# Optimization experiments

Measured on AMD Instinct MI355X. Metric: run time of the kernel, lower is better.

## Reference

```python
import jax, jax.numpy as jnp
import numpy as np

K = 512      # per-token feature dim (also per-head dim in this module)
H = 8        # heads
B = 2
T = 2048


def setup_inputs() -> dict:
    key = jax.random.key(0)
    ks = jax.random.split(key, 6)
    s = 1.0 / np.sqrt(K)
    x = jax.random.normal(ks[0], (B, T, K), dtype=jnp.float32)
    # torch Linear(k, k*heads, bias=False): y = x @ W with W stored here as [in, out]
    Wq = jax.random.uniform(ks[1], (K, K * H), dtype=jnp.float32, minval=-s, maxval=s)
    Wk = jax.random.uniform(ks[2], (K, K * H), dtype=jnp.float32, minval=-s, maxval=s)
    Wv = jax.random.uniform(ks[3], (K, K * H), dtype=jnp.float32, minval=-s, maxval=s)
    su = 1.0 / np.sqrt(K * H)
    Wu = jax.random.uniform(ks[4], (K * H, K), dtype=jnp.float32, minval=-su, maxval=su)
    bu = jax.random.uniform(ks[5], (K,), dtype=jnp.float32, minval=-su, maxval=su)
    return {"x": x, "Wq": Wq, "Wk": Wk, "Wv": Wv, "Wu": Wu, "bu": bu}


def reference(x, Wq, Wk, Wv, Wu, bu):
    b, t, k = x.shape
    h = H
    # project and split heads: [b, t, h, k] -> [b, h, t, k]
    q = (x @ Wq).reshape(b, t, h, k).transpose(0, 2, 1, 3)
    kk = (x @ Wk).reshape(b, t, h, k).transpose(0, 2, 1, 3)
    v = (x @ Wv).reshape(b, t, h, k).transpose(0, 2, 1, 3)
    scale = k ** (-0.25)  # applied to both q and k, matching source
    dot = jnp.einsum('bhqd,bhkd->bhqk', q * scale, kk * scale)
    attn = jax.nn.softmax(dot, axis=-1)
    out = jnp.einsum('bhqk,bhkd->bhqd', attn, v)          # [b, h, t, k]
    out = out.transpose(0, 2, 1, 3).reshape(b, t, h * k)   # [b, t, h*k]
    return out @ Wu + bu
```

## Files before the change

### kernel.cpp

```cpp
#include <hip/hip_runtime.h>

typedef unsigned short u16;
typedef unsigned short ushort8 __attribute__((ext_vector_type(8)));
typedef unsigned short us4 __attribute__((ext_vector_type(4)));
typedef __bf16 bf16x8 __attribute__((ext_vector_type(8)));
typedef float f32x4 __attribute__((ext_vector_type(4)));

#define DEV static __device__ __forceinline__

DEV u16 f2bf(float f) {
    unsigned int u = __builtin_bit_cast(unsigned int, f);
    u += 0x7FFFu + ((u >> 16) & 1u);
    return (u16)(u >> 16);
}

DEV f32x4 mfma16(ushort8 a, ushort8 b, f32x4 c) {
    return __builtin_amdgcn_mfma_f32_16x16x32_bf16((bf16x8)a, (bf16x8)b, c, 0, 0, 0);
}

DEV void gload_lds16(const void* g, void* l) {
    __builtin_amdgcn_global_load_lds(
        (const __attribute__((address_space(1))) void*)g,
        (__attribute__((address_space(3))) void*)l, 16, 0, 0);
}

__global__ void prep_kernel(const float* __restrict__ x,
                            const float* __restrict__ Wq, const float* __restrict__ Wk,
                            const float* __restrict__ Wv, const float* __restrict__ Wu,
                            u16* __restrict__ xb, u16* __restrict__ Wqt, u16* __restrict__ Wut) {
    __shared__ u16 tile[64][72];
    const int bid = blockIdx.x;

    if (bid < 2048) {
        int i = (bid * 256 + threadIdx.x) * 4;
        float4 f = *(const float4*)(x + i);
        us4 o;
        o.x = f2bf(f.x); o.y = f2bf(f.y); o.z = f2bf(f.z); o.w = f2bf(f.w);
        *(us4*)(xb + i) = o;
        return;
    }

    const float* in;
    u16* out;
    int R, C, c0, r0;
    if (bid < 3584) {
        int j = bid - 2048;
        int z = j >> 9, rem = j & 511;
        in = (z == 0) ? Wq : (z == 1) ? Wk : Wv;
        out = Wqt + (size_t)z * 2097152;
        R = 512; C = 4096;
        c0 = (rem & 63) << 6; r0 = (rem >> 6) << 6;
    } else {
        int k = bid - 3584;
        in = Wu; out = Wut;
        R = 4096; C = 512;
        c0 = (k & 7) << 6; r0 = (k >> 3) << 6;
    }
    int tx = threadIdx.x & 63, ty = threadIdx.x >> 6;
    for (int i = 0; i < 64; i += 4) {
        int r = i + ty;
        tile[r][tx] = f2bf(in[(size_t)(r0 + r) * C + c0 + tx]);
    }
    __syncthreads();
    for (int i = 0; i < 64; i += 4) {
        int r = i + ty;
        out[(size_t)(c0 + r) * R + r0 + tx] = tile[tx][r];
    }
}

__launch_bounds__(256, 3)
__global__ void gemm_qkv(const u16* __restrict__ A, const u16* __restrict__ Btbase,
                         float s2, u16* __restrict__ outbase, u16* __restrict__ vtb) {
    __shared__ u16 Asub[128 * 32];
    __shared__ u16 Bsub[128 * 32];
    const int Kc = 512;
    const u16* Bt = Btbase + (size_t)blockIdx.z * 2097152;
    u16* out = outbase + (size_t)blockIdx.z * 16777216;
    const float scale = (blockIdx.z == 0) ? s2 : 1.0f;

    const int tid = threadIdx.x, lane = tid & 63, wv = tid >> 6;
    const int bm = blockIdx.y << 7, bn = blockIdx.x << 7;
    const int wr = (wv >> 1) << 6, wc = (wv & 1) << 6;
    const int lr = lane & 15, hi = lane >> 4;

    f32x4 acc[4][4] = {};

    int off0 = (wv * 2048 + lane * 16) >> 1;
    int row0 = off0 >> 5, k0e = off0 & 31;
    int off1 = off0 + 512;
    int row1 = off1 >> 5, k1e = off1 & 31;

    const u16* Ag0 = A + (size_t)(bm + row0) * Kc + k0e;
    const u16* Ag1 = A + (size_t)(bm + row1) * Kc + k1e;
    const u16* Bg0 = Bt + (size_t)(bn + row0) * Kc + k0e;
    const u16* Bg1 = Bt + (size_t)(bn + row1) * Kc + k1e;

    for (int kk = 0; kk < Kc; kk += 32) {
        __syncthreads();
        gload_lds16(Ag0 + kk, &Asub[wv * 1024]);
        gload_lds16(Ag1 + kk, &Asub[wv * 1024 + 512]);
        gload_lds16(Bg0 + kk, &Bsub[wv * 1024]);
        gload_lds16(Bg1 + kk, &Bsub[wv * 1024 + 512]);
        __syncthreads();

        ushort8 a[4], b[4];
#pragma unroll
        for (int m = 0; m < 4; ++m)
            a[m] = *(const ushort8*)&Asub[(wr + m * 16 + lr) * 32 + hi * 8];
#pragma unroll
        for (int n = 0; n < 4; ++n)
            b[n] = *(const ushort8*)&Bsub[(wc + n * 16 + lr) * 32 + hi * 8];
#pragma unroll
        for (int m = 0; m < 4; ++m)
#pragma unroll
            for (int n = 0; n < 4; ++n)
                acc[m][n] = mfma16(a[m], b[n], acc[m][n]);
    }

    if (blockIdx.z == 2) {
#pragma unroll
        for (int m = 0; m < 4; ++m)
#pragma unroll
            for (int n = 0; n < 4; ++n) {
                int row0v = bm + wr + m * 16 + hi * 4;
                int col   = bn + wc + n * 16 + lr;
                int b = row0v >> 11, t0 = row0v & 2047;
                int h = col >> 9, d = col & 511;
                us4 pk;
#pragma unroll
                for (int r = 0; r < 4; ++r) pk[r] = f2bf(acc[m][n][r]);
                *(us4*)&vtb[(((size_t)(b * 8 + h) * 512 + d) << 11) + t0] = pk;
            }
    } else {
#pragma unroll
        for (int m = 0; m < 4; ++m)
#pragma unroll
            for (int n = 0; n < 4; ++n)
#pragma unroll
                for (int r = 0; r < 4; ++r) {
                    int row = bm + wr + m * 16 + hi * 4 + r;
                    int col = bn + wc + n * 16 + lr;
                    float v = acc[m][n][r] * scale;
                    size_t dst = ((size_t)((row >> 11) * 8 + (col >> 9)) * 2048 + (row & 2047)) * 512
                                 + (col & 511);
                    out[dst] = f2bf(v);
                }
    }
}

__launch_bounds__(256, 3)
__global__ void gemm_final(const u16* __restrict__ A, const u16* __restrict__ Bt,
                           const float* __restrict__ bias, float* __restrict__ out, int Kc) {
    __shared__ u16 Asub[128 * 32];
    __shared__ u16 Bsub[64 * 32];
    const int tid = threadIdx.x, lane = tid & 63, wv = tid >> 6;
    const int bm = blockIdx.y << 7, bn = blockIdx.x << 6;
    const int wr = (wv >> 1) << 6, wc = (wv & 1) << 5;
    const int lr = lane & 15, hi = lane >> 4;

    f32x4 acc[4][2] = {};

    const u16* gsrc[3];
    u16* ldst[3];
#pragma unroll
    for (int j = 0; j < 3; ++j) {
        int g = wv * 3 + j;
        int off = g * 512 + lane * 8;
        if (g < 8) {
            int row = off >> 5, k = off & 31;
            gsrc[j] = A + (size_t)(bm + row) * Kc + k;
            ldst[j] = &Asub[g * 512];
        } else {
            int off2 = off - 4096;
            int row = off2 >> 5, k = off2 & 31;
            gsrc[j] = Bt + (size_t)(bn + row) * Kc + k;
            ldst[j] = &Bsub[(g - 8) * 512];
        }
    }

    for (int kk = 0; kk < Kc; kk += 32) {
        __syncthreads();
#pragma unroll
        for (int j = 0; j < 3; ++j) gload_lds16(gsrc[j] + kk, ldst[j]);
        __syncthreads();

        ushort8 a[4], b[2];
#pragma unroll
        for (int m = 0; m < 4; ++m)
            a[m] = *(const ushort8*)&Asub[(wr + m * 16 + lr) * 32 + hi * 8];
#pragma unroll
        for (int n = 0; n < 2; ++n)
            b[n] = *(const ushort8*)&Bsub[(wc + n * 16 + lr) * 32 + hi * 8];
#pragma unroll
        for (int m = 0; m < 4; ++m)
#pragma unroll
            for (int n = 0; n < 2; ++n)
                acc[m][n] = mfma16(a[m], b[n], acc[m][n]);
    }

#pragma unroll
    for (int m = 0; m < 4; ++m)
#pragma unroll
        for (int n = 0; n < 2; ++n)
#pragma unroll
            for (int r = 0; r < 4; ++r) {
                int row = bm + wr + m * 16 + hi * 4 + r;
                int col = bn + wc + n * 16 + lr;
                out[(size_t)row * 512 + col] = acc[m][n][r] + bias[col];
            }
}

__launch_bounds__(512, 2)
__global__ void attn_kernel(const u16* __restrict__ Q, const u16* __restrict__ K,
                            const u16* __restrict__ Vt, u16* __restrict__ O) {
    __shared__ u16 Klds[2][32 * 512];
    __shared__ u16 Plds[2][128 * 40];
    __shared__ __align__(16) float red[2][128];
    __shared__ __align__(16) float lred[128];
    __shared__ int rflag[2][8];

    const int tid = threadIdx.x, lane = tid & 63, wv = tid >> 6;
    const int lr = lane & 15, hi = lane >> 4;
    const int qh = wv >> 2, ds = wv & 3;

    const int flat = blockIdx.x;
    const int nid = (flat & 7) * 32 + (flat >> 3);
    const int bh = nid >> 4;
    const int q0 = (nid & 15) << 7;

    ushort8 qf[16];
    {
        const char* Qg = (const char*)(Q + ((size_t)bh * 2048 + q0 + wv * 16 + lr) * 512) + hi * 16;
#pragma unroll
        for (int ks = 0; ks < 16; ++ks) qf[ks] = *(const ushort8*)(Qg + ks * 64);
    }

    f32x4 acc[4][8] = {};
    float mrun = -1e30f, lrun = 0.f;

    const char* Kg = (const char*)(K + (size_t)bh * 2048 * 512);
    const char* Vg = (const char*)(Vt + (size_t)bh * 512 * 2048);

    auto s_phase = [&](const char* Kb, f32x4& s0, f32x4& s1) {
        s0 = (f32x4){0.f, 0.f, 0.f, 0.f};
        s1 = (f32x4){0.f, 0.f, 0.f, 0.f};
#pragma unroll
        for (int ks = 0; ks < 16; ++ks) {
            int swz = (ks * 64 + hi * 16) ^ ((lr & 7) << 4);
            ushort8 kf0 = *(const ushort8*)(Kb + lr * 1024 + swz);
            ushort8 kf1 = *(const ushort8*)(Kb + (lr + 16) * 1024 + swz);
            s0 = mfma16(kf0, qf[ks], s0);
            s1 = mfma16(kf1, qf[ks], s1);
        }
    };

    auto softmax_store = [&](const f32x4& s0, const f32x4& s1, int pcb) {
        float mx = fmaxf(fmaxf(fmaxf(s0[0], s0[1]), fmaxf(s0[2], s0[3])),
                         fmaxf(fmaxf(s1[0], s1[1]), fmaxf(s1[2], s1[3])));
        mx = fmaxf(mx, __shfl_xor(mx, 16));
        mx = fmaxf(mx, __shfl_xor(mx, 32));
        float a = 1.0f;
        bool upd = false;
        if (mx > mrun + 11.5f) { a = exp2f(mrun - mx); mrun = mx; upd = true; }
        float p[8];
#pragma unroll
        for (int r = 0; r < 4; ++r) {
            p[r]     = exp2f(s0[r] - mrun);
            p[4 + r] = exp2f(s1[r] - mrun);
        }
        float ps = ((p[0] + p[1]) + (p[2] + p[3])) + ((p[4] + p[5]) + (p[6] + p[7]));
        ps += __shfl_xor(ps, 16);
        ps += __shfl_xor(ps, 32);
        lrun = lrun * a + ps;

        const int qr = wv * 16 + lr;
        char* Pb = (char*)&Plds[pcb][0] + qr * 80;
        uint2 w01, w23;
        w01.x = (unsigned)f2bf(p[0]) | ((unsigned)f2bf(p[1]) << 16);
        w01.y = (unsigned)f2bf(p[2]) | ((unsigned)f2bf(p[3]) << 16);
        w23.x = (unsigned)f2bf(p[4]) | ((unsigned)f2bf(p[5]) << 16);
        w23.y = (unsigned)f2bf(p[6]) | ((unsigned)f2bf(p[7]) << 16);
        *(uint2*)(Pb + hi * 8) = w01;
        *(uint2*)(Pb + 32 + hi * 8) = w23;
        if (hi == 0) red[pcb][qr] = a;
        if (lane == 0) rflag[pcb][wv] = __any(upd) ? 1 : 0;
    };

    auto pv_phase = [&](int pcb, int ktv) {
        int anyupd = rflag[pcb][0] | rflag[pcb][1] | rflag[pcb][2] | rflag[pcb][3]
                   | rflag[pcb][4] | rflag[pcb][5] | rflag[pcb][6] | rflag[pcb][7];
        if (anyupd) {
#pragma unroll
            for (int mf = 0; mf < 4; ++mf) {
                f32x4 a4 = *(const f32x4*)&red[pcb][qh * 64 + mf * 16 + hi * 4];
#pragma unroll
                for (int nf = 0; nf < 8; ++nf)
#pragma unroll
                    for (int r = 0; r < 4; ++r) acc[mf][nf][r] *= a4[r];
            }
        }
        ushort8 pf[4];
#pragma unroll
        for (int mf = 0; mf < 4; ++mf)
            pf[mf] = *(const ushort8*)((const char*)&Plds[pcb][0]
                                       + (qh * 64 + mf * 16 + lr) * 80 + hi * 16);
        __builtin_amdgcn_s_setprio(1);
#pragma unroll
        for (int nf = 0; nf < 8; ++nf) {
            int d = ds * 128 + nf * 16 + lr;
            ushort8 vf = *(const ushort8*)(Vg + (size_t)d * 4096 + (size_t)ktv * 2 + hi * 16);
#pragma unroll
            for (int mf = 0; mf < 4; ++mf) acc[mf][nf] = mfma16(pf[mf], vf, acc[mf][nf]);
        }
        __builtin_amdgcn_s_setprio(0);
    };

    auto prefetch_k = [&](int tt) {
        const char* Kgt = Kg + (size_t)tt * 32 * 1024;
#pragma unroll
        for (int r4 = 0; r4 < 4; ++r4) {
            int r = wv * 4 + r4;
            gload_lds16(Kgt + (size_t)r * 1024 + ((lane ^ (r & 7)) << 4),
                        &Klds[tt & 1][(size_t)r * 512]);
        }
    };

    f32x4 s0c, s1c, s0p, s1p;

    prefetch_k(0);
    __syncthreads();

    prefetch_k(1);
    s_phase((const char*)&Klds[0][0], s0c, s1c);
    __syncthreads();

    for (int t = 1; t < 64; ++t) {
        if (t + 1 < 64) prefetch_k(t + 1);

        s0p = s0c; s1p = s1c;
        s_phase((const char*)&Klds[t & 1][0], s0c, s1c);
        softmax_store(s0p, s1p, (t - 1) & 1);

        __syncthreads();

        pv_phase((t - 1) & 1, (t - 1) << 5);
    }

    softmax_store(s0c, s1c, 1);
    __syncthreads();
    pv_phase(1, 63 << 5);

    if (hi == 0) lred[wv * 16 + lr] = lrun;
    __syncthreads();

    const int b = bh >> 3, h = bh & 7;
#pragma unroll
    for (int mf = 0; mf < 4; ++mf) {
        f32x4 lv = *(const f32x4*)&lred[qh * 64 + mf * 16 + hi * 4];
        f32x4 inv;
#pragma unroll
        for (int r = 0; r < 4; ++r) inv[r] = 1.0f / lv[r];
#pragma unroll
        for (int nf = 0; nf < 8; ++nf) {
            int d = ds * 128 + nf * 16 + lr;
#pragma unroll
            for (int r = 0; r < 4; ++r) {
                int t = q0 + qh * 64 + mf * 16 + hi * 4 + r;
                O[((size_t)(b * 2048 + t)) * 4096 + h * 512 + d] = f2bf(acc[mf][nf][r] * inv[r]);
            }
        }
    }
}

extern "C" void kernel_launch(void* const* d_in, const int* in_sizes, int n_in,
                              void* d_out, int out_size, void* d_ws, size_t ws_size,
                              hipStream_t stream) {
    const float* x  = (const float*)d_in[0];
    const float* Wq = (const float*)d_in[1];
    const float* Wk = (const float*)d_in[2];
    const float* Wv = (const float*)d_in[3];
    const float* Wu = (const float*)d_in[4];
    const float* bu = (const float*)d_in[5];

    char* ws = (char*)d_ws;
    const size_t MB = 1ull << 20;
    u16* xb  = (u16*)(ws + 0);
    u16* Wqt = (u16*)(ws + 4 * MB);
    u16* Wut = (u16*)(ws + 16 * MB);
    u16* Qb  = (u16*)(ws + 20 * MB);
    u16* Kb  = (u16*)(ws + 52 * MB);
    u16* Vtb = (u16*)(ws + 116 * MB);
    u16* Ob  = (u16*)(ws + 84 * MB);

    prep_kernel<<<4096, 256, 0, stream>>>(x, Wq, Wk, Wv, Wu, xb, Wqt, Wut);

    const float s2 = 0.06375871593f;
    gemm_qkv<<<dim3(32, 32, 3), 256, 0, stream>>>(xb, Wqt, s2, Qb, Vtb);

    attn_kernel<<<256, 512, 0, stream>>>(Qb, Kb, Vtb, Ob);

    gemm_final<<<dim3(8, 32), 256, 0, stream>>>(Ob, Wut, bu, (float*)d_out, 4096);
}
```

Baseline: 457.0 us.

## Interleave QK^T MFMAs of the next tile with PV MFMAs of the previous tile

Restructures the attention main loop so each iteration first runs the softmax for the previous score tile, then takes one barrier, then runs a fused phase. The fused phase alternates the QK^T MFMAs for the current K tile with the PV MFMAs and V loads for the previous tile. The aim is to give the MFMA pipe independent work to hide LDS and global V load latency within a single instruction stream. In exchange, softmax no longer overlaps with the score MFMAs and now sits on the critical path before the barrier, and register pressure rises in the fused loop.

```diff
diff --git a/kernel.cpp b/kernel.cpp
--- a/kernel.cpp
+++ b/kernel.cpp
@@ -237,26 +237,37 @@
 
     f32x4 acc[4][8] = {};
     float mrun = -1e30f, lrun = 0.f;
+    f32x4 s0c, s1c;
 
     const char* Kg = (const char*)(K + (size_t)bh * 2048 * 512);
     const char* Vg = (const char*)(Vt + (size_t)bh * 512 * 2048);
 
-    auto s_phase = [&](const char* Kb, f32x4& s0, f32x4& s1) {
-        s0 = (f32x4){0.f, 0.f, 0.f, 0.f};
-        s1 = (f32x4){0.f, 0.f, 0.f, 0.f};
+    auto prefetch_k = [&](int tt) {
+        const char* Kgt = Kg + (size_t)tt * 32 * 1024;
+#pragma unroll
+        for (int r4 = 0; r4 < 4; ++r4) {
+            int r = wv * 4 + r4;
+            gload_lds16(Kgt + (size_t)r * 1024 + ((lane ^ (r & 7)) << 4),
+                        &Klds[tt & 1][(size_t)r * 512]);
+        }
+    };
+
+    auto s_phase = [&](const char* Kb) {
+        s0c = (f32x4){0.f, 0.f, 0.f, 0.f};
+        s1c = (f32x4){0.f, 0.f, 0.f, 0.f};
 #pragma unroll
         for (int ks = 0; ks < 16; ++ks) {
             int swz = (ks * 64 + hi * 16) ^ ((lr & 7) << 4);
             ushort8 kf0 = *(const ushort8*)(Kb + lr * 1024 + swz);
             ushort8 kf1 = *(const ushort8*)(Kb + (lr + 16) * 1024 + swz);
-            s0 = mfma16(kf0, qf[ks], s0);
-            s1 = mfma16(kf1, qf[ks], s1);
+            s0c = mfma16(kf0, qf[ks], s0c);
+            s1c = mfma16(kf1, qf[ks], s1c);
         }
     };
 
-    auto softmax_store = [&](const f32x4& s0, const f32x4& s1, int pcb) {
-        float mx = fmaxf(fmaxf(fmaxf(s0[0], s0[1]), fmaxf(s0[2], s0[3])),
-                         fmaxf(fmaxf(s1[0], s1[1]), fmaxf(s1[2], s1[3])));
+    auto softmax_store = [&](int pcb) {
+        float mx = fmaxf(fmaxf(fmaxf(s0c[0], s0c[1]), fmaxf(s0c[2], s0c[3])),
+                         fmaxf(fmaxf(s1c[0], s1c[1]), fmaxf(s1c[2], s1c[3])));
         mx = fmaxf(mx, __shfl_xor(mx, 16));
         mx = fmaxf(mx, __shfl_xor(mx, 32));
         float a = 1.0f;
@@ -265,8 +276,8 @@
         float p[8];
 #pragma unroll
         for (int r = 0; r < 4; ++r) {
-            p[r]     = exp2f(s0[r] - mrun);
-            p[4 + r] = exp2f(s1[r] - mrun);
+            p[r]     = exp2f(s0c[r] - mrun);
+            p[4 + r] = exp2f(s1c[r] - mrun);
         }
         float ps = ((p[0] + p[1]) + (p[2] + p[3])) + ((p[4] + p[5]) + (p[6] + p[7]));
         ps += __shfl_xor(ps, 16);
@@ -286,6 +297,50 @@
         if (lane == 0) rflag[pcb][wv] = __any(upd) ? 1 : 0;
     };
 
+    auto fused_phase = [&](int t, int pcb, int ktv) {
+        int anyupd = rflag[pcb][0] | rflag[pcb][1] | rflag[pcb][2] | rflag[pcb][3]
+                   | rflag[pcb][4] | rflag[pcb][5] | rflag[pcb][6] | rflag[pcb][7];
+        if (anyupd) {
+#pragma unroll
+            for (int mf = 0; mf < 4; ++mf) {
+                f32x4 a4 = *(const f32x4*)&red[pcb][qh * 64 + mf * 16 + hi * 4];
+#pragma unroll
+                for (int nf = 0; nf < 8; ++nf)
+#pragma unroll
+                    for (int r = 0; r < 4; ++r) acc[mf][nf][r] *= a4[r];
+            }
+        }
+        ushort8 pf[4];
+#pragma unroll
+        for (int mf = 0; mf < 4; ++mf)
+            pf[mf] = *(const ushort8*)((const char*)&Plds[pcb][0]
+                                       + (qh * 64 + mf * 16 + lr) * 80 + hi * 16);
+        const char* Kb = (const char*)&Klds[t & 1][0];
+        s0c = (f32x4){0.f, 0.f, 0.f, 0.f};
+        s1c = (f32x4){0.f, 0.f, 0.f, 0.f};
+        ushort8 vf;
+        __builtin_amdgcn_s_setprio(1);
+#pragma unroll
+        for (int ks = 0; ks < 16; ++ks) {
+            int swz = (ks * 64 + hi * 16) ^ ((lr & 7) << 4);
+            ushort8 kf0 = *(const ushort8*)(Kb + lr * 1024 + swz);
+            ushort8 kf1 = *(const ushort8*)(Kb + (lr + 16) * 1024 + swz);
+            if ((ks & 1) == 0) {
+                int nf = ks >> 1;
+                int d = ds * 128 + nf * 16 + lr;
+                vf = *(const ushort8*)(Vg + (size_t)d * 4096 + (size_t)ktv * 2 + hi * 16);
+            }
+            s0c = mfma16(kf0, qf[ks], s0c);
+            s1c = mfma16(kf1, qf[ks], s1c);
+            if (ks & 1) {
+                int nf = ks >> 1;
+#pragma unroll
+                for (int mf = 0; mf < 4; ++mf) acc[mf][nf] = mfma16(pf[mf], vf, acc[mf][nf]);
+            }
+        }
+        __builtin_amdgcn_s_setprio(0);
+    };
+
     auto pv_phase = [&](int pcb, int ktv) {
         int anyupd = rflag[pcb][0] | rflag[pcb][1] | rflag[pcb][2] | rflag[pcb][3]
                    | rflag[pcb][4] | rflag[pcb][5] | rflag[pcb][6] | rflag[pcb][7];
@@ -304,7 +359,6 @@
         for (int mf = 0; mf < 4; ++mf)
             pf[mf] = *(const ushort8*)((const char*)&Plds[pcb][0]
                                        + (qh * 64 + mf * 16 + lr) * 80 + hi * 16);
-        __builtin_amdgcn_s_setprio(1);
 #pragma unroll
         for (int nf = 0; nf < 8; ++nf) {
             int d = ds * 128 + nf * 16 + lr;
@@ -312,41 +366,21 @@
 #pragma unroll
             for (int mf = 0; mf < 4; ++mf) acc[mf][nf] = mfma16(pf[mf], vf, acc[mf][nf]);
         }
-        __builtin_amdgcn_s_setprio(0);
     };
-
-    auto prefetch_k = [&](int tt) {
-        const char* Kgt = Kg + (size_t)tt * 32 * 1024;
-#pragma unroll
-        for (int r4 = 0; r4 < 4; ++r4) {
-            int r = wv * 4 + r4;
-            gload_lds16(Kgt + (size_t)r * 1024 + ((lane ^ (r & 7)) << 4),
-                        &Klds[tt & 1][(size_t)r * 512]);
-        }
-    };
-
-    f32x4 s0c, s1c, s0p, s1p;
 
     prefetch_k(0);
     __syncthreads();
-
     prefetch_k(1);
-    s_phase((const char*)&Klds[0][0], s0c, s1c);
-    __syncthreads();
+    s_phase((const char*)&Klds[0][0]);
 
     for (int t = 1; t < 64; ++t) {
+        softmax_store((t - 1) & 1);
+        __syncthreads();
         if (t + 1 < 64) prefetch_k(t + 1);
-
-        s0p = s0c; s1p = s1c;
-        s_phase((const char*)&Klds[t & 1][0], s0c, s1c);
-        softmax_store(s0p, s1p, (t - 1) & 1);
-
-        __syncthreads();
-
-        pv_phase((t - 1) & 1, (t - 1) << 5);
-    }
-
-    softmax_store(s0c, s1c, 1);
+        fused_phase(t, (t - 1) & 1, (t - 1) << 5);
+    }
+
+    softmax_store(1);
     __syncthreads();
     pv_phase(1, 63 << 5);
 
```

New measurement: 499.7 us. 1.09x slower.
